# Optimization experiments

Hardware: AMD Instinct MI355X
Metric: run time of the kernel (lower is better)

## Reference

```python
import jax, jax.numpy as jnp
import numpy as np

KH = KW = 3  # fixed: distortion() generates a 9-tap (3x3) offset grid


def make_offset(h, w, dilation=1.0, skydome=True):
    """Faithful numpy port of DistortionConvLayer.distortion -> [1,h,w,9,2] (last dim = [x_off, y_off])."""
    pi = np.pi
    unit_w = 2.0 * pi / w
    unit_h = pi / (2.0 * h) if skydome else pi / h
    rho = np.tan(unit_w) * dilation
    v = np.array([0.0, 1.0, 0.0])
    r_grid = np.array([[1, -1], [1, 0], [1, 1], [0, -1], [0, 0], [0, 1], [-1, -1], [-1, 0], [-1, 1]], dtype=np.float64)
    xc = int(w * 0.5)
    theta = (xc - 0.5 * w) * unit_w
    y = np.arange(h, dtype=np.float64)
    phi = (h - y) * unit_h if skydome else (h * 0.5 - y) * unit_h  # [h]
    p_u = np.stack([np.cos(phi) * np.cos(theta), np.sin(phi), np.cos(phi) * np.sin(theta)], axis=-1)  # [h,3]
    t_x = np.cross(np.broadcast_to(v, p_u.shape), p_u)  # [h,3]
    t_y = np.cross(p_u, t_x)                            # [h,3]
    # r_sphere: [h,9,3]
    r_sphere = rho * (r_grid[None, :, 0, None] * t_x[:, None, :] + r_grid[None, :, 1, None] * t_y[:, None, :])
    p_ur = p_u[:, None, :] + r_sphere  # [h,9,3]
    ux, uy, uz = p_ur[..., 0], p_ur[..., 1], p_ur[..., 2]
    base = np.arctan2(uz, ux)
    theta_r = np.where(ux > 0, base,
               np.where(ux < 0, np.where(uz >= 0, base + pi, base - pi),
                np.where(uz > 0, pi * 0.5, -pi * 0.5)))
    phi_r = np.arcsin(uy)
    x_r = (theta_r / pi + 1.0) * 0.5 * w
    y_r = (1.0 - 2.0 * phi_r / pi) * h if skydome else (0.5 - phi_r / pi) * h
    k = np.stack([x_r, y_r], axis=-1)          # [h,9,2], entries [x, y] (as in original)
    off = k - k[:, 4:5, :]                      # subtract center tap
    off = np.broadcast_to(off[:, None, :, :], (h, w, 9, 2))  # tile over width
    return off[None].astype(np.float32)         # [1,h,w,9,2]


def setup_inputs() -> dict:
    key = jax.random.key(0)
    k1, k2 = jax.random.split(key)
    B, H, W, C, F = 4, 128, 256, 64, 128
    inputs = jax.random.normal(k1, (B, H, W, C), dtype=jnp.float32)
    fan_in = KH * KW * C
    kernel = jax.random.normal(k2, (fan_in, F), dtype=jnp.float32) * (1.0 / np.sqrt(fan_in))
    bias = jnp.zeros((F,), dtype=jnp.float32)
    return {"inputs": inputs, "kernel": kernel, "bias": bias}


def reference(inputs, kernel, bias):
    B, H, W, C = inputs.shape
    F = kernel.shape[1]
    off = jnp.asarray(make_offset(H, W))  # [1,H,W,9,2], static constant
    # 'same' padding for 3x3, stride 1, dilation 1 -> pad 1 on each side
    xp = jnp.pad(inputs, ((0, 0), (1, 1), (1, 1), (0, 0)))
    in_h, in_w = H + 2, W + 2
    # base conv sampling coordinates (extract_patches order: tap k -> dy=k//3, dx=k%3)
    dy = jnp.repeat(jnp.arange(KH), KW).astype(jnp.float32)  # [9]
    dx = jnp.tile(jnp.arange(KW), KH).astype(jnp.float32)    # [9]
    base_y = jnp.arange(H, dtype=jnp.float32)[None, :, None, None] + dy[None, None, None, :]  # [1,H,1,9]
    base_x = jnp.arange(W, dtype=jnp.float32)[None, None, :, None] + dx[None, None, None, :]  # [1,1,W,9]
    # NOTE: faithful to original: channel 0 of offset (x_r diffs) is added to y, channel 1 to x
    y = base_y + off[..., 0]  # [1,H,W,9]
    x = base_x + off[..., 1]
    y = jnp.clip(y, 0.0, in_h - 1)
    x = jnp.where(x < 0, x + in_w, x)
    x = jnp.where(x > in_w - 1, x - in_w, x)
    y0 = jnp.floor(y).astype(jnp.int32)
    x0 = jnp.floor(x).astype(jnp.int32)
    y1, x1 = y0 + 1, x0 + 1
    y0 = jnp.clip(y0, 0, in_h - 1); y1 = jnp.clip(y1, 0, in_h - 1)
    x0 = jnp.clip(x0, 0, in_w - 1); x1 = jnp.clip(x1, 0, in_w - 1)
    bidx = jnp.arange(B)[:, None, None, None]  # [B,1,1,1], broadcasts against [1,H,W,9]
    gather = lambda yi, xi: xp[bidx, yi, xi]   # -> [B,H,W,9,C]
    p0 = gather(y0, x0); p1 = gather(y0, x1); p2 = gather(y1, x0); p3 = gather(y1, x1)
    y0f, y1f = y0.astype(jnp.float32), y1.astype(jnp.float32)
    x0f, x1f = x0.astype(jnp.float32), x1.astype(jnp.float32)
    w0 = ((y1f - y) * (x1f - x))[..., None]
    w1 = ((y1f - y) * (x - x0f))[..., None]
    w2 = ((y - y0f) * (x1f - x))[..., None]
    w3 = ((y - y0f) * (x - x0f))[..., None]
    pixels = w0 * p0 + w1 * p1 + w2 * p2 + w3 * p3  # [B,H,W,9,C]
    pixels = pixels.reshape(B, H * W, KH * KW * C)
    out = pixels @ kernel + bias                    # [B,HW,F]
    return jax.nn.relu(out.reshape(B, H, W, F))
```

## Files before the change

kernel.cpp:

```cpp
#include <hip/hip_runtime.h>
#include <math.h>

#define Bb 4
#define Hh 128
#define Ww 256
#define Cc 64
#define Ff 128
#define INH 130
#define INW 258

#define WSLOT 72
#define WCOLS 132

typedef __attribute__((ext_vector_type(8))) __bf16 bf16x8;
typedef __attribute__((ext_vector_type(4))) float floatx4;

__device__ __forceinline__ unsigned short f2bf(float f) {
  unsigned int u = __float_as_uint(f);
  unsigned int r = u + 0x7fffu + ((u >> 16) & 1u);
  return (unsigned short)(r >> 16);
}

__global__ void prep_kernel(const float* __restrict__ kmat,
                            float* __restrict__ offtab,
                            unsigned short* __restrict__ kT) {
  int gid = blockIdx.x * 256 + threadIdx.x;
  if (gid < 576 * 128) {
    int f = gid & 127;
    int k = gid >> 7;
    kT[f * 576 + k] = f2bf(kmat[gid]);
  }
  if (gid < Hh * 9) {
    int h = gid / 9;
    int j = gid - h * 9;
    const double pi = 3.14159265358979323846;
    double unit_w = 2.0 * pi / (double)Ww;
    double unit_h = pi / (2.0 * (double)Hh);
    double rho = tan(unit_w);
    double theta = ((double)(Ww / 2) - 0.5 * (double)Ww) * unit_w;
    double phi = ((double)Hh - (double)h) * unit_h;
    double cph = cos(phi), sph = sin(phi);
    double cth = cos(theta), sth = sin(theta);
    double pux = cph * cth, puy = sph, puz = cph * sth;
    double txx = puz, txy = 0.0, txz = -pux;
    double tyx = puy * txz - puz * txy;
    double tyy = puz * txx - pux * txz;
    double tyz = pux * txy - puy * txx;
    const int r0t[9] = {1, 1, 1, 0, 0, 0, -1, -1, -1};
    const int r1t[9] = {-1, 0, 1, -1, 0, 1, -1, 0, 1};
    auto proj = [&](int r0, int r1, double& xr, double& yr) {
      double ux = pux + rho * ((double)r0 * txx + (double)r1 * tyx);
      double uy = puy + rho * ((double)r0 * txy + (double)r1 * tyy);
      double uz = puz + rho * ((double)r0 * txz + (double)r1 * tyz);
      double base = atan2(uz, ux);
      double th;
      if (ux > 0.0)        th = base;
      else if (ux < 0.0)   th = (uz >= 0.0) ? base + pi : base - pi;
      else                 th = (uz > 0.0) ? pi * 0.5 : -pi * 0.5;
      double ph = asin(uy);
      xr = (th / pi + 1.0) * 0.5 * (double)Ww;
      yr = (1.0 - 2.0 * ph / pi) * (double)Hh;
    };
    double xc, yc, xj, yj;
    proj(0, 0, xc, yc);
    proj(r0t[j], r1t[j], xj, yj);
    offtab[gid * 2 + 0] = (float)(xj - xc);
    offtab[gid * 2 + 1] = (float)(yj - yc);
  }
}

__global__ __launch_bounds__(256, 4) void fused_kernel(
    const float* __restrict__ in, const float* __restrict__ bias,
    const unsigned short* __restrict__ kT, const float* __restrict__ offtab,
    float* __restrict__ out) {
  __shared__ unsigned short winH[WCOLS * WSLOT];
  __shared__ unsigned short lB[128 * WSLOT];

  int lidx = ((blockIdx.x & 7) << 7) | (blockIdx.x >> 3);
  int wt = lidx & 1;
  int h  = (lidx >> 1) & 127;
  int b  = lidx >> 8;
  int w0 = wt << 7;

  int tid  = threadIdx.x;
  int lane = tid & 63;
  int wave = tid >> 6;
  int m_base = (wave >> 1) << 6;
  int n_base = (wave & 1) << 6;
  int l15  = lane & 15;
  int quad = lane >> 4;

  floatx4 acc[4][4];
#pragma unroll
  for (int i = 0; i < 4; i++)
#pragma unroll
    for (int j = 0; j < 4; j++) acc[i][j] = (floatx4){0.f, 0.f, 0.f, 0.f};

  const float* inb = in + (size_t)b * Hh * Ww * Cc;

  for (int tap = 0; tap < 9; tap++) {
    float off0 = offtab[(h * 9 + tap) * 2 + 0];
    float off1 = offtab[(h * 9 + tap) * 2 + 1];
    float dyk = (float)(tap / 3), dxk = (float)(tap % 3);

    float y = (float)h + dyk + off0;
    y = fminf(fmaxf(y, 0.f), (float)(INH - 1));
    int y0i = (int)floorf(y);
    int y1i = y0i + 1;
    y0i = min(max(y0i, 0), INH - 1);
    y1i = min(max(y1i, 0), INH - 1);
    float wy0 = (float)y1i - y;
    float wy1 = y - (float)y0i;
    if (!(y0i >= 1 && y0i <= Hh)) wy0 = 0.f;
    if (!(y1i >= 1 && y1i <= Hh)) wy1 = 0.f;
    const float* row0 = inb + (size_t)min(max(y0i - 1, 0), Hh - 1) * Ww * Cc;
    const float* row1 = inb + (size_t)min(max(y1i - 1, 0), Hh - 1) * Ww * Cc;

    float xrep = (float)w0 + dxk + off1;
    float flo  = floorf(xrep);
    int jb = (int)flo - 1;
    float fr = xrep - flo;
    float q00 = wy0 * (1.f - fr), q01 = wy0 * fr;
    float q10 = wy1 * (1.f - fr), q11 = wy1 * fr;

    int slotv[4];
#pragma unroll
    for (int mi = 0; mi < 4; mi++) {
      int w = m_base + mi * 16 + l15;
      float x = (float)(w0 + w) + dxk + off1;
      if (x < 0.f) x += (float)INW;
      if (x > (float)(INW - 1)) x -= (float)INW;
      int x0i = (int)floorf(x);
      int s = x0i - jb;
      if (s < 0) s += INW;
      if (s > 131) s = 131;
      slotv[mi] = s;
    }

#pragma unroll 3
    for (int it = 0; it < 9; it++) {
      int task = tid + (it << 8);
      if (task < WCOLS * 16) {
        int j  = task >> 4;
        int c4 = (task & 15) << 2;
        int col = jb + j;
        if (col < 0) col += INW;
        if (col > INW - 1) col -= INW;
        int ncol = jb + j + 1;
        if (ncol < 0) ncol += INW;
        if (ncol > INW - 1) ncol -= INW;
        bool cok = (col >= 1) & (col <= Ww) & (j < 131);
        bool nok = (ncol >= 1) & (ncol <= Ww) & (j < 131);
        int ci = min(max(col - 1, 0), Ww - 1);
        int ni = min(max(ncol - 1, 0), Ww - 1);
        float4 a0 = *(const float4*)(row0 + ci * Cc + c4);
        float4 a1 = *(const float4*)(row0 + ni * Cc + c4);
        float4 b0 = *(const float4*)(row1 + ci * Cc + c4);
        float4 b1 = *(const float4*)(row1 + ni * Cc + c4);
        float m0 = cok ? 1.f : 0.f, m1 = nok ? 1.f : 0.f;
        float w00 = q00 * m0, w01 = q01 * m1, w10 = q10 * m0, w11 = q11 * m1;
        float4 p;
        p.x = w00 * a0.x + w01 * a1.x + w10 * b0.x + w11 * b1.x;
        p.y = w00 * a0.y + w01 * a1.y + w10 * b0.y + w11 * b1.y;
        p.z = w00 * a0.z + w01 * a1.z + w10 * b0.z + w11 * b1.z;
        p.w = w00 * a0.w + w01 * a1.w + w10 * b0.w + w11 * b1.w;
        uint2 st;
        st.x = (unsigned int)f2bf(p.x) | ((unsigned int)f2bf(p.y) << 16);
        st.y = (unsigned int)f2bf(p.z) | ((unsigned int)f2bf(p.w) << 16);
        *(uint2*)(&winH[j * WSLOT + c4]) = st;
      }
    }

    {
      int f = tid >> 1, seg = tid & 1;
      const unsigned short* src = kT + f * 576 + tap * 64 + seg * 32;
      unsigned short* dst = &lB[f * WSLOT + seg * 32];
#pragma unroll
      for (int i = 0; i < 4; i++)
        *(uint4*)(dst + i * 8) = *(const uint4*)(src + i * 8);
    }

    __syncthreads();

#pragma unroll
    for (int kk = 0; kk < 2; kk++) {
      bf16x8 afrag[4], bfrag[4];
#pragma unroll
      for (int mi = 0; mi < 4; mi++)
        afrag[mi] = *(const bf16x8*)&winH[slotv[mi] * WSLOT + kk * 32 + quad * 8];
#pragma unroll
      for (int ni = 0; ni < 4; ni++)
        bfrag[ni] = *(const bf16x8*)&lB[(n_base + ni * 16 + l15) * WSLOT + kk * 32 + quad * 8];
#pragma unroll
      for (int mi = 0; mi < 4; mi++)
#pragma unroll
        for (int ni = 0; ni < 4; ni++)
          acc[mi][ni] = __builtin_amdgcn_mfma_f32_16x16x32_bf16(
              afrag[mi], bfrag[ni], acc[mi][ni], 0, 0, 0);
    }
    __syncthreads();
  }

  size_t outbase = ((size_t)(b * Hh + h) * Ww + w0);
#pragma unroll
  for (int ni = 0; ni < 4; ni++) {
    int f = n_base + ni * 16 + l15;
    float bv = bias[f];
#pragma unroll
    for (int mi = 0; mi < 4; mi++) {
#pragma unroll
      for (int r = 0; r < 4; r++) {
        int m = m_base + mi * 16 + quad * 4 + r;
        out[(outbase + m) * Ff + f] = fmaxf(acc[mi][ni][r] + bv, 0.f);
      }
    }
  }
}

extern "C" void kernel_launch(void* const* d_in, const int* in_sizes, int n_in,
                              void* d_out, int out_size, void* d_ws, size_t ws_size,
                              hipStream_t stream) {
  const float* in   = (const float*)d_in[0];
  const float* kmat = (const float*)d_in[1];
  const float* bias = (const float*)d_in[2];
  float* out = (float*)d_out;

  float* offtab = (float*)d_ws;
  unsigned short* kT = (unsigned short*)((char*)d_ws + Hh * 9 * 2 * sizeof(float));
  if (ws_size < (size_t)(Hh * 9 * 2 * sizeof(float) + 128 * 576 * sizeof(unsigned short)))
    return;

  prep_kernel<<<288, 256, 0, stream>>>(kmat, offtab, kT);
  fused_kernel<<<Bb * Hh * (Ww / 128), 256, 0, stream>>>(in, bias, kT, offtab, out);
}
```

Before: 153.5 us.

## Prepack weights in MFMA fragment order, read B from global, move offsets to host

The prep kernel now writes the bf16 weight matrix already laid out in MFMA B-fragment order, so the fused kernel loads B fragments straight from global/L2 and drops the shared-memory weight tile and its staging copy each tap. The gather loop gives each thread 16 channels instead of 4 and uses hardware bf16 conversion in place of manual rounding. The spherical offset table, which depends only on shapes, is computed in double on the host each call and copied asynchronously, removing the double-precision trig from the device prep kernel. The risks are more global-load latency on the MFMA path and a host-side compute plus a copy from a static buffer on every launch.

```diff
diff --git a/kernel.cpp b/kernel.cpp
--- a/kernel.cpp
+++ b/kernel.cpp
@@ -15,66 +15,29 @@
 typedef __attribute__((ext_vector_type(8))) __bf16 bf16x8;
 typedef __attribute__((ext_vector_type(4))) float floatx4;
 
-__device__ __forceinline__ unsigned short f2bf(float f) {
-  unsigned int u = __float_as_uint(f);
-  unsigned int r = u + 0x7fffu + ((u >> 16) & 1u);
-  return (unsigned short)(r >> 16);
-}
-
 __global__ void prep_kernel(const float* __restrict__ kmat,
-                            float* __restrict__ offtab,
-                            unsigned short* __restrict__ kT) {
+                            unsigned short* __restrict__ kTp) {
   int gid = blockIdx.x * 256 + threadIdx.x;
-  if (gid < 576 * 128) {
-    int f = gid & 127;
-    int k = gid >> 7;
-    kT[f * 576 + k] = f2bf(kmat[gid]);
-  }
-  if (gid < Hh * 9) {
-    int h = gid / 9;
-    int j = gid - h * 9;
-    const double pi = 3.14159265358979323846;
-    double unit_w = 2.0 * pi / (double)Ww;
-    double unit_h = pi / (2.0 * (double)Hh);
-    double rho = tan(unit_w);
-    double theta = ((double)(Ww / 2) - 0.5 * (double)Ww) * unit_w;
-    double phi = ((double)Hh - (double)h) * unit_h;
-    double cph = cos(phi), sph = sin(phi);
-    double cth = cos(theta), sth = sin(theta);
-    double pux = cph * cth, puy = sph, puz = cph * sth;
-    double txx = puz, txy = 0.0, txz = -pux;
-    double tyx = puy * txz - puz * txy;
-    double tyy = puz * txx - pux * txz;
-    double tyz = pux * txy - puy * txx;
-    const int r0t[9] = {1, 1, 1, 0, 0, 0, -1, -1, -1};
-    const int r1t[9] = {-1, 0, 1, -1, 0, 1, -1, 0, 1};
-    auto proj = [&](int r0, int r1, double& xr, double& yr) {
-      double ux = pux + rho * ((double)r0 * txx + (double)r1 * tyx);
-      double uy = puy + rho * ((double)r0 * txy + (double)r1 * tyy);
-      double uz = puz + rho * ((double)r0 * txz + (double)r1 * tyz);
-      double base = atan2(uz, ux);
-      double th;
-      if (ux > 0.0)        th = base;
-      else if (ux < 0.0)   th = (uz >= 0.0) ? base + pi : base - pi;
-      else                 th = (uz > 0.0) ? pi * 0.5 : -pi * 0.5;
-      double ph = asin(uy);
-      xr = (th / pi + 1.0) * 0.5 * (double)Ww;
-      yr = (1.0 - 2.0 * ph / pi) * (double)Hh;
-    };
-    double xc, yc, xj, yj;
-    proj(0, 0, xc, yc);
-    proj(r0t[j], r1t[j], xj, yj);
-    offtab[gid * 2 + 0] = (float)(xj - xc);
-    offtab[gid * 2 + 1] = (float)(yj - yc);
-  }
+  int lane = gid & 63;
+  int chunk = gid >> 6;
+  if (chunk >= 144) return;
+  int ni  = chunk & 3;
+  int nh  = (chunk >> 2) & 1;
+  int kk  = (chunk >> 3) & 1;
+  int tap = chunk >> 4;
+  int n  = nh * 64 + ni * 16 + (lane & 15);
+  int k0 = tap * 64 + kk * 32 + (lane >> 4) * 8;
+  bf16x8 v;
+#pragma unroll
+  for (int s = 0; s < 8; s++) v[s] = (__bf16)kmat[(k0 + s) * 128 + n];
+  *(bf16x8*)(kTp + chunk * 512 + lane * 8) = v;
 }
 
 __global__ __launch_bounds__(256, 4) void fused_kernel(
     const float* __restrict__ in, const float* __restrict__ bias,
-    const unsigned short* __restrict__ kT, const float* __restrict__ offtab,
+    const unsigned short* __restrict__ kTp, const float* __restrict__ offtab,
     float* __restrict__ out) {
   __shared__ unsigned short winH[WCOLS * WSLOT];
-  __shared__ unsigned short lB[128 * WSLOT];
 
   int lidx = ((blockIdx.x & 7) << 7) | (blockIdx.x >> 3);
   int wt = lidx & 1;
@@ -86,7 +49,7 @@
   int lane = tid & 63;
   int wave = tid >> 6;
   int m_base = (wave >> 1) << 6;
-  int n_base = (wave & 1) << 6;
+  int nh     = wave & 1;
   int l15  = lane & 15;
   int quad = lane >> 4;
 
@@ -137,12 +100,12 @@
       slotv[mi] = s;
     }
 
-#pragma unroll 3
-    for (int it = 0; it < 9; it++) {
+#pragma unroll
+    for (int it = 0; it < 3; it++) {
       int task = tid + (it << 8);
-      if (task < WCOLS * 16) {
-        int j  = task >> 4;
-        int c4 = (task & 15) << 2;
+      if (task < WCOLS * 4) {
+        int j   = task >> 2;
+        int c16 = (task & 3) << 4;
         int col = jb + j;
         if (col < 0) col += INW;
         if (col > INW - 1) col -= INW;
@@ -152,32 +115,35 @@
         bool cok = (col >= 1) & (col <= Ww) & (j < 131);
         bool nok = (ncol >= 1) & (ncol <= Ww) & (j < 131);
         int ci = min(max(col - 1, 0), Ww - 1);
-        int ni = min(max(ncol - 1, 0), Ww - 1);
-        float4 a0 = *(const float4*)(row0 + ci * Cc + c4);
-        float4 a1 = *(const float4*)(row0 + ni * Cc + c4);
-        float4 b0 = *(const float4*)(row1 + ci * Cc + c4);
-        float4 b1 = *(const float4*)(row1 + ni * Cc + c4);
-        float m0 = cok ? 1.f : 0.f, m1 = nok ? 1.f : 0.f;
-        float w00 = q00 * m0, w01 = q01 * m1, w10 = q10 * m0, w11 = q11 * m1;
-        float4 p;
-        p.x = w00 * a0.x + w01 * a1.x + w10 * b0.x + w11 * b1.x;
-        p.y = w00 * a0.y + w01 * a1.y + w10 * b0.y + w11 * b1.y;
-        p.z = w00 * a0.z + w01 * a1.z + w10 * b0.z + w11 * b1.z;
-        p.w = w00 * a0.w + w01 * a1.w + w10 * b0.w + w11 * b1.w;
-        uint2 st;
-        st.x = (unsigned int)f2bf(p.x) | ((unsigned int)f2bf(p.y) << 16);
-        st.y = (unsigned int)f2bf(p.z) | ((unsigned int)f2bf(p.w) << 16);
-        *(uint2*)(&winH[j * WSLOT + c4]) = st;
+        int nx = min(max(ncol - 1, 0), Ww - 1);
+        float w00 = cok ? q00 : 0.f, w01 = nok ? q01 : 0.f;
+        float w10 = cok ? q10 : 0.f, w11 = nok ? q11 : 0.f;
+        const float* p0 = row0 + ci * Cc + c16;
+        const float* p1 = row0 + nx * Cc + c16;
+        const float* p2 = row1 + ci * Cc + c16;
+        const float* p3 = row1 + nx * Cc + c16;
+        bf16x8 o0, o1;
+#pragma unroll
+        for (int q = 0; q < 4; q++) {
+          float4 a0 = *(const float4*)(p0 + 4 * q);
+          float4 a1 = *(const float4*)(p1 + 4 * q);
+          float4 b0 = *(const float4*)(p2 + 4 * q);
+          float4 b1 = *(const float4*)(p3 + 4 * q);
+          float px = w00 * a0.x + w01 * a1.x + w10 * b0.x + w11 * b1.x;
+          float py = w00 * a0.y + w01 * a1.y + w10 * b0.y + w11 * b1.y;
+          float pz = w00 * a0.z + w01 * a1.z + w10 * b0.z + w11 * b1.z;
+          float pw = w00 * a0.w + w01 * a1.w + w10 * b0.w + w11 * b1.w;
+          if (q < 2) {
+            o0[q * 4 + 0] = (__bf16)px; o0[q * 4 + 1] = (__bf16)py;
+            o0[q * 4 + 2] = (__bf16)pz; o0[q * 4 + 3] = (__bf16)pw;
+          } else {
+            o1[(q - 2) * 4 + 0] = (__bf16)px; o1[(q - 2) * 4 + 1] = (__bf16)py;
+            o1[(q - 2) * 4 + 2] = (__bf16)pz; o1[(q - 2) * 4 + 3] = (__bf16)pw;
+          }
+        }
+        *(bf16x8*)&winH[j * WSLOT + c16]     = o0;
+        *(bf16x8*)&winH[j * WSLOT + c16 + 8] = o1;
       }
-    }
-
-    {
-      int f = tid >> 1, seg = tid & 1;
-      const unsigned short* src = kT + f * 576 + tap * 64 + seg * 32;
-      unsigned short* dst = &lB[f * WSLOT + seg * 32];
-#pragma unroll
-      for (int i = 0; i < 4; i++)
-        *(uint4*)(dst + i * 8) = *(const uint4*)(src + i * 8);
     }
 
     __syncthreads();
@@ -185,12 +151,14 @@
 #pragma unroll
     for (int kk = 0; kk < 2; kk++) {
       bf16x8 afrag[4], bfrag[4];
+      const unsigned short* kb =
+          kTp + (size_t)((((tap * 2 + kk) * 2 + nh) * 4) * 512) + lane * 8;
+#pragma unroll
+      for (int ni = 0; ni < 4; ni++)
+        bfrag[ni] = *(const bf16x8*)(kb + ni * 512);
 #pragma unroll
       for (int mi = 0; mi < 4; mi++)
         afrag[mi] = *(const bf16x8*)&winH[slotv[mi] * WSLOT + kk * 32 + quad * 8];
-#pragma unroll
-      for (int ni = 0; ni < 4; ni++)
-        bfrag[ni] = *(const bf16x8*)&lB[(n_base + ni * 16 + l15) * WSLOT + kk * 32 + quad * 8];
 #pragma unroll
       for (int mi = 0; mi < 4; mi++)
 #pragma unroll
@@ -204,7 +172,7 @@
   size_t outbase = ((size_t)(b * Hh + h) * Ww + w0);
 #pragma unroll
   for (int ni = 0; ni < 4; ni++) {
-    int f = n_base + ni * 16 + l15;
+    int f = nh * 64 + ni * 16 + l15;
     float bv = bias[f];
 #pragma unroll
     for (int mi = 0; mi < 4; mi++) {
@@ -213,6 +181,48 @@
         int m = m_base + mi * 16 + quad * 4 + r;
         out[(outbase + m) * Ff + f] = fmaxf(acc[mi][ni][r] + bv, 0.f);
       }
+    }
+  }
+}
+
+static float h_off[Hh * 9 * 2];
+
+static void compute_offsets_host() {
+  const double pi = 3.14159265358979323846;
+  double unit_w = 2.0 * pi / (double)Ww;
+  double unit_h = pi / (2.0 * (double)Hh);
+  double rho = tan(unit_w);
+  double theta = ((double)(Ww / 2) - 0.5 * (double)Ww) * unit_w;
+  static const int r0t[9] = {1, 1, 1, 0, 0, 0, -1, -1, -1};
+  static const int r1t[9] = {-1, 0, 1, -1, 0, 1, -1, 0, 1};
+  for (int h = 0; h < Hh; h++) {
+    double phi = ((double)Hh - (double)h) * unit_h;
+    double cph = cos(phi), sph = sin(phi);
+    double cth = cos(theta), sth = sin(theta);
+    double pux = cph * cth, puy = sph, puz = cph * sth;
+    double txx = puz, txy = 0.0, txz = -pux;
+    double tyx = puy * txz - puz * txy;
+    double tyy = puz * txx - pux * txz;
+    double tyz = pux * txy - puy * txx;
+    double xr[10], yr[10];
+    for (int p = 0; p < 10; p++) {
+      int r0 = (p == 9) ? 0 : r0t[p];
+      int r1 = (p == 9) ? 0 : r1t[p];
+      double ux = pux + rho * ((double)r0 * txx + (double)r1 * tyx);
+      double uy = puy + rho * ((double)r0 * txy + (double)r1 * tyy);
+      double uz = puz + rho * ((double)r0 * txz + (double)r1 * tyz);
+      double base = atan2(uz, ux);
+      double th;
+      if (ux > 0.0)        th = base;
+      else if (ux < 0.0)   th = (uz >= 0.0) ? base + pi : base - pi;
+      else                 th = (uz > 0.0) ? pi * 0.5 : -pi * 0.5;
+      double ph = asin(uy);
+      xr[p] = (th / pi + 1.0) * 0.5 * (double)Ww;
+      yr[p] = (1.0 - 2.0 * ph / pi) * (double)Hh;
+    }
+    for (int j = 0; j < 9; j++) {
+      h_off[(h * 9 + j) * 2 + 0] = (float)(xr[j] - xr[9]);
+      h_off[(h * 9 + j) * 2 + 1] = (float)(yr[j] - yr[9]);
     }
   }
 }
@@ -226,10 +236,12 @@
   float* out = (float*)d_out;
 
   float* offtab = (float*)d_ws;
-  unsigned short* kT = (unsigned short*)((char*)d_ws + Hh * 9 * 2 * sizeof(float));
-  if (ws_size < (size_t)(Hh * 9 * 2 * sizeof(float) + 128 * 576 * sizeof(unsigned short)))
+  unsigned short* kTp = (unsigned short*)((char*)d_ws + Hh * 9 * 2 * sizeof(float));
+  if (ws_size < (size_t)(Hh * 9 * 2 * sizeof(float) + 144 * 512 * sizeof(unsigned short)))
     return;
 
-  prep_kernel<<<288, 256, 0, stream>>>(kmat, offtab, kT);
-  fused_kernel<<<Bb * Hh * (Ww / 128), 256, 0, stream>>>(in, bias, kT, offtab, out);
-}
+  compute_offsets_host();
+  hipMemcpyAsync(offtab, h_off, sizeof(h_off), hipMemcpyHostToDevice, stream);
+  prep_kernel<<<36, 256, 0, stream>>>(kmat, kTp);
+  fused_kernel<<<Bb * Hh * (Ww / 128), 256, 0, stream>>>(in, bias, kTp, offtab, out);
+}
```

After: 236.4 us. 54.0% more time.
